# Performance work log

Measured on AMD Instinct MI355X. Metric: run time of the kernel, lower is better.

## Reference

```python
import jax, jax.numpy as jnp
import numpy as np

E, K, H, I = 16, 4, 2048, 1024
B, S = 1, 2048


def setup_inputs() -> dict:
    key = jax.random.key(0)
    ks = jax.random.split(key, 5)
    scale_in = 1.0 / np.sqrt(H)
    scale_mid = 1.0 / np.sqrt(I)
    return {
        "x": jax.random.normal(ks[0], (B, S, H), dtype=jnp.float32),
        "gate_w": jax.random.normal(ks[1], (E, H), dtype=jnp.float32) * scale_in,
        "w1_gate": jax.random.normal(ks[2], (E, I, H), dtype=jnp.float32) * scale_in,
        "w1_up": jax.random.normal(ks[3], (E, I, H), dtype=jnp.float32) * scale_in,
        "w2": jax.random.normal(ks[4], (E, H, I), dtype=jnp.float32) * scale_mid,
        "topk": K,
    }


def reference(x, gate_w, w1_gate, w1_up, w2, topk):
    orig_shape = x.shape
    xt = x.reshape(-1, x.shape[-1])            # [T, H]
    T = xt.shape[0]
    n_exp = gate_w.shape[0]

    # Router: top-k logits, softmax over the selected k (as in the torch code).
    logits = xt @ gate_w.T                      # [T, E]
    topk_vals, topk_ids = jax.lax.top_k(logits, topk)
    topk_w = jax.nn.softmax(topk_vals, axis=-1)  # [T, K]

    # Dense per-token-per-expert combine weight; 0 for unselected experts.
    # Mathematically identical to the gather/scatter-add loop: unselected
    # experts contribute expert_out * 0.
    gate_dense = jnp.zeros((T, n_exp), dtype=xt.dtype)
    gate_dense = gate_dense.at[jnp.arange(T)[:, None], topk_ids].add(topk_w)

    # SwiGLU per expert (dense over experts; weights zero-out unused ones).
    g = jnp.einsum("th,eih->tei", xt, w1_gate)   # [T, E, I]
    u = jnp.einsum("th,eih->tei", xt, w1_up)     # [T, E, I]
    h = jax.nn.silu(g) * u                        # [T, E, I]
    out = jnp.einsum("tei,te,ehi->th", h, gate_dense, w2)  # [T, H]
    return out.reshape(orig_shape)
```

## Files before the change

### kernel.cpp

```cpp
#include <hip/hip_runtime.h>
#include <hip/hip_bf16.h>
#include <stdint.h>

#define NEXP 16
#define KSEL 4
#define HDIM 2048
#define IDIM 1024
#define TTOK 2048
#define NT1 16
#define NTB 16
#define MAXT1 80
#define MAXB1 (MAXT1 * NT1)
#define MAXTB 47
#define MAXBB (MAXTB * NTB)
#define NCVT 1024
#define NCVT1 512
#define NW8 ((NEXP * IDIM * HDIM) / 8)

typedef __attribute__((ext_vector_type(8))) short bf16x8;
typedef __attribute__((ext_vector_type(4))) float f32x4;
typedef unsigned int u32;

__device__ __forceinline__ uint32_t pack2(float a, float b) {
  __hip_bfloat162 h = __float22bfloat162_rn(float2{a, b});
  uint32_t u;
  __builtin_memcpy(&u, &h, 4);
  return u;
}
__device__ __forceinline__ ushort bf1(float a) {
  __hip_bfloat16 h = __float2bfloat16(a);
  ushort u;
  __builtin_memcpy(&u, &h, 2);
  return u;
}
__device__ __forceinline__ void gload16(const void* g, void* l) {
  __builtin_amdgcn_global_load_lds(
      (const __attribute__((address_space(1))) u32*)g,
      (__attribute__((address_space(3))) u32*)l, 16, 0, 0);
}
__device__ __forceinline__ int swzread(int row, int q) {
  return row * 32 + ((q ^ ((row >> 1) & 3)) << 3);
}
__device__ __forceinline__ void cvt_bodyN(const float* __restrict__ src,
                                          ushort* __restrict__ dst,
                                          int idx0, int stride) {
  for (int i = idx0; i < NW8; i += stride) {
    f32x4 a = __builtin_nontemporal_load(((const f32x4*)src) + i * 2);
    f32x4 b = __builtin_nontemporal_load(((const f32x4*)src) + i * 2 + 1);
    uint4 t;
    t.x = pack2(a[0], a[1]); t.y = pack2(a[2], a[3]);
    t.z = pack2(b[0], b[1]); t.w = pack2(b[2], b[3]);
    ((uint4*)dst)[i] = t;
  }
}

__global__ __launch_bounds__(256) void router_kernel(
    const float* __restrict__ x, const float* __restrict__ gw,
    ushort* __restrict__ xb, int* __restrict__ topk_id,
    float* __restrict__ topk_w,
    const float* __restrict__ srcG, ushort* __restrict__ dstG,
    const float* __restrict__ srcU, ushort* __restrict__ dstU)
{
  if (blockIdx.x >= TTOK / 4 + NCVT) {
    cvt_bodyN(srcU, dstU,
              (blockIdx.x - (TTOK / 4 + NCVT)) * 256 + threadIdx.x, NCVT * 256);
    return;
  }
  if (blockIdx.x >= TTOK / 4) {
    cvt_bodyN(srcG, dstG,
              (blockIdx.x - TTOK / 4) * 256 + threadIdx.x, NCVT * 256);
    return;
  }
  const int wid = threadIdx.x >> 6;
  const int lane = threadIdx.x & 63;
  const int t = blockIdx.x * 4 + wid;
  const float4* x4 = (const float4*)(x + (size_t)t * HDIM);
  const float4* gw4 = (const float4*)gw;
  float acc[NEXP];
#pragma unroll
  for (int e = 0; e < NEXP; ++e) acc[e] = 0.f;
#pragma unroll
  for (int i = 0; i < HDIM / 256; ++i) {
    const int idx = i * 64 + lane;
    float4 xv = x4[idx];
    uint2 xp;
    xp.x = pack2(xv.x, xv.y);
    xp.y = pack2(xv.z, xv.w);
    *(uint2*)(xb + (size_t)t * HDIM + idx * 4) = xp;
#pragma unroll
    for (int e = 0; e < NEXP; ++e) {
      float4 wv = gw4[e * (HDIM / 4) + idx];
      acc[e] += xv.x * wv.x + xv.y * wv.y + xv.z * wv.z + xv.w * wv.w;
    }
  }
#pragma unroll
  for (int e = 0; e < NEXP; ++e) {
#pragma unroll
    for (int off = 32; off >= 1; off >>= 1)
      acc[e] += __shfl_xor(acc[e], off);
  }
  if (lane == 0) {
    unsigned taken = 0;
    float vals[KSEL];
    int ids[KSEL];
#pragma unroll
    for (int k = 0; k < KSEL; ++k) {
      float bv = -3.4e38f; int bi = 0;
      for (int e = 0; e < NEXP; ++e)
        if (!((taken >> e) & 1u) && acc[e] > bv) { bv = acc[e]; bi = e; }
      taken |= 1u << bi; vals[k] = bv; ids[k] = bi;
    }
    float m = vals[0], s = 0.f, w[KSEL];
#pragma unroll
    for (int k = 0; k < KSEL; ++k) { w[k] = __expf(vals[k] - m); s += w[k]; }
    float is = 1.f / s;
#pragma unroll
    for (int k = 0; k < KSEL; ++k) {
      topk_id[t * KSEL + k] = ids[k];
      topk_w[t * KSEL + k] = w[k] * is;
    }
  }
}

__global__ __launch_bounds__(1024) void plan_scatter_kernel(
    const int* __restrict__ topk_id, int* __restrict__ counts,
    int* __restrict__ offsets, int* __restrict__ nWA, int* __restrict__ nWB,
    int* __restrict__ wlA, int* __restrict__ wlB,
    int* __restrict__ rowTok, int* __restrict__ inv)
{
  __shared__ int cnt[NEXP], off[NEXP], cur[NEXP];
  __shared__ int t1[NEXP], p1[NEXP], tB[NEXP], pB[NEXP];
  const int tid = threadIdx.x;
  if (tid < NEXP) { cnt[tid] = 0; cur[tid] = 0; }
  __syncthreads();
  for (int i = tid; i < TTOK * KSEL; i += 1024)
    atomicAdd(&cnt[topk_id[i]], 1);
  __syncthreads();
  if (tid == 0) {
    int s = 0, a = 0, b = 0;
    for (int e = 0; e < NEXP; ++e) {
      off[e] = s; s += cnt[e];
      t1[e] = (cnt[e] + 127) >> 7;  p1[e] = a;  a += t1[e];
      tB[e] = (cnt[e] + 255) >> 8;  pB[e] = b;  b += tB[e];
    }
    *nWA = a * NT1;
    *nWB = b * NTB;
  }
  __syncthreads();
  if (tid < NEXP) {
    counts[tid] = cnt[tid];
    offsets[tid] = off[tid];
    const int e = tid, T = t1[e];
    int idx = p1[e] * NT1;
    for (int nt = 0; nt < NT1; ++nt)
      for (int mt = 0; mt < T; ++mt)
        wlA[idx++] = (e << 12) | (nt << 6) | mt;
  } else if (tid < 2 * NEXP) {
    const int e = tid - NEXP, T = tB[e];
    int idx = pB[e] * NTB;
    for (int nt = 0; nt < NTB; ++nt)
      for (int mt = 0; mt < T; ++mt)
        wlB[idx++] = (e << 12) | (nt << 6) | mt;
  }
  for (int i = tid; i < TTOK * KSEL; i += 1024) {
    const int e = topk_id[i];
    const int pos = atomicAdd(&cur[e], 1);
    const int row = off[e] + pos;
    rowTok[row] = i >> 2;
    inv[i] = row;
  }
}

__global__ __launch_bounds__(512) void gemm1_kernel(
    const ushort* __restrict__ xb,
    const ushort* __restrict__ wG, const ushort* __restrict__ wU,
    const int* __restrict__ rowTok, const int* __restrict__ counts,
    const int* __restrict__ offsets, const int* __restrict__ nW,
    const int* __restrict__ wl, ushort* __restrict__ hbuf,
    const float* __restrict__ cvsrc, ushort* __restrict__ cvdst)
{
  if (blockIdx.x >= MAXB1) {
    cvt_bodyN(cvsrc, cvdst,
              (blockIdx.x - MAXB1) * 512 + threadIdx.x, NCVT1 * 512);
    return;
  }
  const int nTot = *nW;
  const int L = (blockIdx.x & 7) * (MAXB1 / 8) + (blockIdx.x >> 3);
  if (L >= nTot) return;
  const int w = wl[L];
  const int e = w >> 12, nt = (w >> 6) & 63, mt = w & 63;
  const int n_e = counts[e], rowbase = offsets[e];

  __shared__ ushort lds[24576];
#define AS(b) (lds + (b) * 4096)
#define BG(b) (lds + 12288 + (b) * 2048)
#define BU(b) (lds + 18432 + (b) * 2048)

  const int tid = threadIdx.x;
  const int lane = tid & 63;
  const int wv = tid >> 6;

  const int arow = tid >> 2;
  const int ckA = tid & 3;
  const int schA = (ckA ^ ((arow >> 1) & 3)) << 3;
  const int agr = mt * 128 + arow;
  const int tokA = rowTok[rowbase + (agr < n_e ? agr : n_e - 1)];
  const ushort* pA = xb + (size_t)tokA * HDIM + schA;
  const int bloc = tid & 255;
  const int brow = bloc >> 2;
  const int ckB = bloc & 3;
  const int schB = (ckB ^ ((brow >> 1) & 3)) << 3;
  const size_t wbase = (size_t)e * IDIM * HDIM;
  const ushort* pB = ((tid < 256) ? wG : wU) + wbase +
                     (size_t)(nt * 64 + brow) * HDIM + schB;

  const int wr = (wv >> 2) << 6;
  const int ng = wv & 3;
  const bool isU = ng >= 2;
  const int wc = (ng & 1) << 5;
  const int lr = lane & 15;
  const int q = lane >> 4;

  f32x4 acc[4][2];
#pragma unroll
  for (int i = 0; i < 4; ++i)
#pragma unroll
    for (int j = 0; j < 2; ++j) acc[i][j] = (f32x4){0.f, 0.f, 0.f, 0.f};

  auto STAGE = [&](int b) {
    gload16(pA, AS(b) + tid * 8);
    if (tid < 256) gload16(pB, BG(b) + bloc * 8);
    else           gload16(pB, BU(b) + bloc * 8);
    pA += 32; pB += 32;
  };

  const int NTK = HDIM / 32;
  STAGE(0);
  STAGE(1);
  asm volatile("s_waitcnt vmcnt(2)" ::: "memory");
  __builtin_amdgcn_s_barrier();
  __builtin_amdgcn_sched_barrier(0);
  int buf = 0;
  for (int kt = 0; kt < NTK; ++kt) {
    if (kt + 2 < NTK) STAGE(buf == 0 ? 2 : buf - 1);
    const ushort* bsrc = isU ? BU(buf) : BG(buf);
    bf16x8 af[4], bf[2];
#pragma unroll
    for (int mi = 0; mi < 4; ++mi)
      af[mi] = *(const bf16x8*)&AS(buf)[swzread(wr + mi * 16 + lr, q)];
#pragma unroll
    for (int ni = 0; ni < 2; ++ni)
      bf[ni] = *(const bf16x8*)&bsrc[swzread(wc + ni * 16 + lr, q)];
#pragma unroll
    for (int mi = 0; mi < 4; ++mi)
#pragma unroll
      for (int ni = 0; ni < 2; ++ni)
        acc[mi][ni] = __builtin_amdgcn_mfma_f32_16x16x32_bf16(af[mi], bf[ni], acc[mi][ni], 0, 0, 0);
    if (kt + 1 < NTK) {
      if (kt + 2 < NTK)
        asm volatile("s_waitcnt vmcnt(2)" ::: "memory");
      else
        asm volatile("s_waitcnt vmcnt(0)" ::: "memory");
      __builtin_amdgcn_s_barrier();
      __builtin_amdgcn_sched_barrier(0);
    }
    buf = (buf == 2) ? 0 : buf + 1;
  }

  __syncthreads();
  float* uex = (float*)lds;
  if (isU) {
    const int ucol0 = ((ng - 2) << 5);
#pragma unroll
    for (int mi = 0; mi < 4; ++mi)
#pragma unroll
      for (int ni = 0; ni < 2; ++ni)
#pragma unroll
        for (int r = 0; r < 4; ++r)
          uex[(wr + mi * 16 + q * 4 + r) * 64 + ucol0 + ni * 16 + lr] = acc[mi][ni][r];
  }
  __syncthreads();
  if (!isU) {
    const int gcol0 = (ng << 5);
#pragma unroll
    for (int mi = 0; mi < 4; ++mi)
#pragma unroll
      for (int ni = 0; ni < 2; ++ni) {
        const int lcol = gcol0 + ni * 16 + lr;
        const int col = nt * 64 + lcol;
#pragma unroll
        for (int r = 0; r < 4; ++r) {
          const int lrow = wr + mi * 16 + q * 4 + r;
          const int mrow = mt * 128 + lrow;
          if (mrow < n_e) {
            const float gv = acc[mi][ni][r];
            const float uv = uex[lrow * 64 + lcol];
            const float hv = (gv / (1.f + __expf(-gv))) * uv;
            hbuf[(size_t)(rowbase + mrow) * IDIM + col] = bf1(hv);
          }
        }
      }
  }
#undef AS
#undef BG
#undef BU
}

__global__ __launch_bounds__(512) void gemmB_kernel(
    const ushort* __restrict__ hb, const ushort* __restrict__ wb,
    const int* __restrict__ counts, const int* __restrict__ offsets,
    const int* __restrict__ nW, const int* __restrict__ wl,
    ushort* __restrict__ po)
{
  const int nTot = *nW;
  const int L = (blockIdx.x & 7) * (MAXBB / 8) + (blockIdx.x >> 3);
  if (L >= nTot) return;
  const int w = wl[L];
  const int e = w >> 12, nt = (w >> 6) & 63, mt = w & 63;
  const int n_e = counts[e], rowbase = offsets[e];

  __shared__ ushort As[2][256 * 32];
  __shared__ ushort Bs[2][128 * 32];

  const int tid = threadIdx.x;
  const int lane = tid & 63;
  const int wid = tid >> 6;

  const int lr4 = lane >> 2;
  const int ckA = lane & 3;
  const int arl0 = wid * 32 + lr4;
  const int arl1 = wid * 32 + 16 + lr4;
  const int schA0 = (ckA ^ ((arl0 >> 1) & 3)) << 3;
  const int schA1 = (ckA ^ ((arl1 >> 1) & 3)) << 3;
  const int ag0 = mt * 256 + arl0, ag1 = mt * 256 + arl1;
  const int g0 = rowbase + (ag0 < n_e ? ag0 : n_e - 1);
  const int g1 = rowbase + (ag1 < n_e ? ag1 : n_e - 1);
  const ushort* pA0 = hb + (size_t)g0 * IDIM + schA0;
  const ushort* pA1 = hb + (size_t)g1 * IDIM + schA1;
  const int brl = wid * 16 + lr4;
  const int schB = (ckA ^ ((brl >> 1) & 3)) << 3;
  const size_t wbase = (size_t)e * HDIM * IDIM;
  const ushort* pB = wb + wbase + (size_t)(nt * 128 + brl) * IDIM + schB;

  const int wr = (wid >> 1) << 6;
  const int wc = (wid & 1) << 6;
  const int lr = lane & 15;
  const int q = lane >> 4;

  f32x4 acc[4][4];
#pragma unroll
  for (int i = 0; i < 4; ++i)
#pragma unroll
    for (int j = 0; j < 4; ++j) acc[i][j] = (f32x4){0.f, 0.f, 0.f, 0.f};

  auto STAGE = [&](int b) {
    gload16(pA0, &As[b][wid * 1024 + lane * 8]);
    gload16(pA1, &As[b][wid * 1024 + 512 + lane * 8]);
    gload16(pB, &Bs[b][wid * 512 + lane * 8]);
    pA0 += 32; pA1 += 32; pB += 32;
  };

  const int NTK = IDIM / 32;
  STAGE(0);
  __syncthreads();
  int buf = 0;
  for (int kt = 0; kt < NTK; ++kt) {
    if (kt + 1 < NTK) STAGE(buf ^ 1);
    bf16x8 af[4], bfr[4];
#pragma unroll
    for (int mi = 0; mi < 4; ++mi)
      af[mi] = *(const bf16x8*)&As[buf][swzread(wr + mi * 16 + lr, q)];
#pragma unroll
    for (int ni = 0; ni < 4; ++ni)
      bfr[ni] = *(const bf16x8*)&Bs[buf][swzread(wc + ni * 16 + lr, q)];
#pragma unroll
    for (int mi = 0; mi < 4; ++mi)
#pragma unroll
      for (int ni = 0; ni < 4; ++ni)
        acc[mi][ni] = __builtin_amdgcn_mfma_f32_16x16x32_bf16(af[mi], bfr[ni], acc[mi][ni], 0, 0, 0);
    __syncthreads();
    buf ^= 1;
  }

#pragma unroll
  for (int mi = 0; mi < 4; ++mi) {
#pragma unroll
    for (int ni = 0; ni < 4; ++ni) {
      const int col = nt * 128 + wc + ni * 16 + lr;
#pragma unroll
      for (int r = 0; r < 4; ++r) {
        const int mrow = mt * 256 + wr + mi * 16 + q * 4 + r;
        if (mrow < n_e)
          po[(size_t)(rowbase + mrow) * HDIM + col] = bf1(acc[mi][ni][r]);
      }
    }
  }
}

__global__ __launch_bounds__(256) void combine_kernel(
    const ushort* __restrict__ po, const int* __restrict__ inv,
    const float* __restrict__ tw, float* __restrict__ out)
{
  const int t = blockIdx.x;
  const int r0 = inv[t * 4 + 0], r1 = inv[t * 4 + 1];
  const int r2 = inv[t * 4 + 2], r3 = inv[t * 4 + 3];
  const float w0 = tw[t * 4 + 0], w1 = tw[t * 4 + 1];
  const float w2v = tw[t * 4 + 2], w3 = tw[t * 4 + 3];
  const int i = threadIdx.x;
  uint4 v0 = *(const uint4*)(po + (size_t)r0 * HDIM + i * 8);
  uint4 v1 = *(const uint4*)(po + (size_t)r1 * HDIM + i * 8);
  uint4 v2 = *(const uint4*)(po + (size_t)r2 * HDIM + i * 8);
  uint4 v3 = *(const uint4*)(po + (size_t)r3 * HDIM + i * 8);
  float o[8];
#pragma unroll
  for (int w = 0; w < 4; ++w) {
    const uint32_t a = (&v0.x)[w], b = (&v1.x)[w], c = (&v2.x)[w], d = (&v3.x)[w];
    o[w * 2 + 0] = w0 * __builtin_bit_cast(float, a << 16) +
                   w1 * __builtin_bit_cast(float, b << 16) +
                   w2v * __builtin_bit_cast(float, c << 16) +
                   w3 * __builtin_bit_cast(float, d << 16);
    o[w * 2 + 1] = w0 * __builtin_bit_cast(float, a & 0xffff0000u) +
                   w1 * __builtin_bit_cast(float, b & 0xffff0000u) +
                   w2v * __builtin_bit_cast(float, c & 0xffff0000u) +
                   w3 * __builtin_bit_cast(float, d & 0xffff0000u);
  }
  float4* o4 = (float4*)(out + (size_t)t * HDIM + i * 8);
  o4[0] = (float4){o[0], o[1], o[2], o[3]};
  o4[1] = (float4){o[4], o[5], o[6], o[7]};
}

extern "C" void kernel_launch(void* const* d_in, const int* in_sizes, int n_in,
                              void* d_out, int out_size, void* d_ws, size_t ws_size,
                              hipStream_t stream) {
  const float* x   = (const float*)d_in[0];
  const float* gw  = (const float*)d_in[1];
  const float* w1g = (const float*)d_in[2];
  const float* w1u = (const float*)d_in[3];
  const float* w2  = (const float*)d_in[4];
  float* out = (float*)d_out;

  char* ws = (char*)d_ws;
  ushort* xb    = (ushort*)(ws + 0);
  ushort* wbufG = (ushort*)(ws + 8388608);
  ushort* wbufU = (ushort*)(ws + 75497472);
  ushort* wbuf2 = (ushort*)(ws + 142606336);
  ushort* hbuf  = (ushort*)(ws + 209715200);
  ushort* po    = (ushort*)(ws + 226492416);
  int*    tkid   = (int*)(ws + 260046848);
  float*  tkw    = (float*)(ws + 260046848 + 32768);
  int*    rowTok = (int*)(ws + 260046848 + 65536);
  int*    inv    = (int*)(ws + 260046848 + 98304);
  int*    ctrl   = (int*)(ws + 260177920);
  int* counts  = ctrl;
  int* offsets = ctrl + 32;
  int* nWA     = ctrl + 50;
  int* nWB     = ctrl + 51;
  int* wlA     = ctrl + 64;
  int* wlB     = ctrl + 64 + MAXB1;

  router_kernel<<<TTOK / 4 + 2 * NCVT, 256, 0, stream>>>(
      x, gw, xb, tkid, tkw, w1g, wbufG, w1u, wbufU);
  plan_scatter_kernel<<<1, 1024, 0, stream>>>(tkid, counts, offsets, nWA, nWB,
                                              wlA, wlB, rowTok, inv);
  gemm1_kernel<<<MAXB1 + NCVT1, 512, 0, stream>>>(
      xb, wbufG, wbufU, rowTok, counts, offsets, nWA, wlA, hbuf,
      w2, wbuf2);
  gemmB_kernel<<<MAXBB, 512, 0, stream>>>(hbuf, wbuf2, counts, offsets,
                                          nWB, wlB, po);
  combine_kernel<<<TTOK, 256, 0, stream>>>(po, inv, tkw, out);
}
```

Before: 309.4 us.

## Convert fp32 gate/up weights to bf16 inside gemm1 instead of separate pass

```diff
diff --git a/kernel.cpp b/kernel.cpp
--- a/kernel.cpp
+++ b/kernel.cpp
@@ -14,7 +14,6 @@
 #define MAXTB 47
 #define MAXBB (MAXTB * NTB)
 #define NCVT 1024
-#define NCVT1 512
 #define NW8 ((NEXP * IDIM * HDIM) / 8)
 
 typedef __attribute__((ext_vector_type(8))) short bf16x8;
@@ -58,16 +57,10 @@
     const float* __restrict__ x, const float* __restrict__ gw,
     ushort* __restrict__ xb, int* __restrict__ topk_id,
     float* __restrict__ topk_w,
-    const float* __restrict__ srcG, ushort* __restrict__ dstG,
-    const float* __restrict__ srcU, ushort* __restrict__ dstU)
+    const float* __restrict__ src2, ushort* __restrict__ dst2)
 {
-  if (blockIdx.x >= TTOK / 4 + NCVT) {
-    cvt_bodyN(srcU, dstU,
-              (blockIdx.x - (TTOK / 4 + NCVT)) * 256 + threadIdx.x, NCVT * 256);
-    return;
-  }
   if (blockIdx.x >= TTOK / 4) {
-    cvt_bodyN(srcG, dstG,
+    cvt_bodyN(src2, dst2,
               (blockIdx.x - TTOK / 4) * 256 + threadIdx.x, NCVT * 256);
     return;
   }
@@ -173,17 +166,11 @@
 
 __global__ __launch_bounds__(512) void gemm1_kernel(
     const ushort* __restrict__ xb,
-    const ushort* __restrict__ wG, const ushort* __restrict__ wU,
+    const float* __restrict__ wG, const float* __restrict__ wU,
     const int* __restrict__ rowTok, const int* __restrict__ counts,
     const int* __restrict__ offsets, const int* __restrict__ nW,
-    const int* __restrict__ wl, ushort* __restrict__ hbuf,
-    const float* __restrict__ cvsrc, ushort* __restrict__ cvdst)
+    const int* __restrict__ wl, ushort* __restrict__ hbuf)
 {
-  if (blockIdx.x >= MAXB1) {
-    cvt_bodyN(cvsrc, cvdst,
-              (blockIdx.x - MAXB1) * 512 + threadIdx.x, NCVT1 * 512);
-    return;
-  }
   const int nTot = *nW;
   const int L = (blockIdx.x & 7) * (MAXB1 / 8) + (blockIdx.x >> 3);
   if (L >= nTot) return;
@@ -206,13 +193,15 @@
   const int agr = mt * 128 + arow;
   const int tokA = rowTok[rowbase + (agr < n_e ? agr : n_e - 1)];
   const ushort* pA = xb + (size_t)tokA * HDIM + schA;
+
   const int bloc = tid & 255;
-  const int brow = bloc >> 2;
+  const int browB = bloc >> 2;
   const int ckB = bloc & 3;
-  const int schB = (ckB ^ ((brow >> 1) & 3)) << 3;
-  const size_t wbase = (size_t)e * IDIM * HDIM;
-  const ushort* pB = ((tid < 256) ? wG : wU) + wbase +
-                     (size_t)(nt * 64 + brow) * HDIM + schB;
+  const int ckW = ckB ^ ((browB >> 1) & 3);
+  const size_t wbaseF = (size_t)e * IDIM * HDIM;
+  const float* pBf = ((tid < 256) ? wG : wU) + wbaseF +
+                     (size_t)(nt * 64 + browB) * HDIM + ckB * 8;
+  const int bofs = browB * 32 + ckW * 8;
 
   const int wr = (wv >> 2) << 6;
   const int ng = wv & 3;
@@ -227,44 +216,96 @@
 #pragma unroll
     for (int j = 0; j < 2; ++j) acc[i][j] = (f32x4){0.f, 0.f, 0.f, 0.f};
 
-  auto STAGE = [&](int b) {
-    gload16(pA, AS(b) + tid * 8);
-    if (tid < 256) gload16(pB, BG(b) + bloc * 8);
-    else           gload16(pB, BU(b) + bloc * 8);
-    pA += 32; pB += 32;
+  auto WRB = [&](int b, const f32x4& va, const f32x4& vb) {
+    uint4 t;
+    t.x = pack2(va[0], va[1]); t.y = pack2(va[2], va[3]);
+    t.z = pack2(vb[0], vb[1]); t.w = pack2(vb[2], vb[3]);
+    ushort* dst = (tid < 256 ? BG(b) : BU(b)) + bofs;
+    *(uint4*)dst = t;
   };
 
   const int NTK = HDIM / 32;
-  STAGE(0);
-  STAGE(1);
-  asm volatile("s_waitcnt vmcnt(2)" ::: "memory");
+  gload16(pA, AS(0) + tid * 8); pA += 32;
+  gload16(pA, AS(1) + tid * 8); pA += 32;
+  f32x4 s0a = *(const f32x4*)(pBf);
+  f32x4 s0b = *(const f32x4*)(pBf + 4);
+  WRB(0, s0a, s0b);
+  f32x4 s1a = *(const f32x4*)(pBf + 32);
+  f32x4 s1b = *(const f32x4*)(pBf + 36);
+  asm volatile("s_waitcnt lgkmcnt(0)" ::: "memory");
   __builtin_amdgcn_s_barrier();
   __builtin_amdgcn_sched_barrier(0);
-  int buf = 0;
-  for (int kt = 0; kt < NTK; ++kt) {
-    if (kt + 2 < NTK) STAGE(buf == 0 ? 2 : buf - 1);
-    const ushort* bsrc = isU ? BU(buf) : BG(buf);
-    bf16x8 af[4], bf[2];
-#pragma unroll
-    for (int mi = 0; mi < 4; ++mi)
-      af[mi] = *(const bf16x8*)&AS(buf)[swzread(wr + mi * 16 + lr, q)];
-#pragma unroll
-    for (int ni = 0; ni < 2; ++ni)
-      bf[ni] = *(const bf16x8*)&bsrc[swzread(wc + ni * 16 + lr, q)];
-#pragma unroll
-    for (int mi = 0; mi < 4; ++mi)
+
+  int cur = 0;
+  for (int t = 0; t < NTK; t += 2) {
+    {
+      const int nxt = (cur == 2) ? 0 : cur + 1;
+      const int nn = (nxt == 2) ? 0 : nxt + 1;
+      if (t + 1 < NTK) WRB(nxt, s1a, s1b);
+      if (t + 2 < NTK) {
+        s0a = *(const f32x4*)(pBf + (t + 2) * 32);
+        s0b = *(const f32x4*)(pBf + (t + 2) * 32 + 4);
+        gload16(pA, AS(nn) + tid * 8); pA += 32;
+      }
+      const ushort* bsrc = isU ? BU(cur) : BG(cur);
+      bf16x8 af[4], bf[2];
+#pragma unroll
+      for (int mi = 0; mi < 4; ++mi)
+        af[mi] = *(const bf16x8*)&AS(cur)[swzread(wr + mi * 16 + lr, q)];
 #pragma unroll
       for (int ni = 0; ni < 2; ++ni)
-        acc[mi][ni] = __builtin_amdgcn_mfma_f32_16x16x32_bf16(af[mi], bf[ni], acc[mi][ni], 0, 0, 0);
-    if (kt + 1 < NTK) {
-      if (kt + 2 < NTK)
-        asm volatile("s_waitcnt vmcnt(2)" ::: "memory");
-      else
-        asm volatile("s_waitcnt vmcnt(0)" ::: "memory");
-      __builtin_amdgcn_s_barrier();
-      __builtin_amdgcn_sched_barrier(0);
-    }
-    buf = (buf == 2) ? 0 : buf + 1;
+        bf[ni] = *(const bf16x8*)&bsrc[swzread(wc + ni * 16 + lr, q)];
+#pragma unroll
+      for (int mi = 0; mi < 4; ++mi)
+#pragma unroll
+        for (int ni = 0; ni < 2; ++ni)
+          acc[mi][ni] = __builtin_amdgcn_mfma_f32_16x16x32_bf16(af[mi], bf[ni], acc[mi][ni], 0, 0, 0);
+      if (t + 1 < NTK) {
+        if (t + 2 < NTK)
+          asm volatile("s_waitcnt vmcnt(3)" ::: "memory");
+        else
+          asm volatile("s_waitcnt vmcnt(0)" ::: "memory");
+        asm volatile("s_waitcnt lgkmcnt(0)" ::: "memory");
+        __builtin_amdgcn_s_barrier();
+        __builtin_amdgcn_sched_barrier(0);
+      }
+      cur = nxt;
+    }
+    {
+      const int u = t + 1;
+      if (u >= NTK) break;
+      const int nxt = (cur == 2) ? 0 : cur + 1;
+      const int nn = (nxt == 2) ? 0 : nxt + 1;
+      if (u + 1 < NTK) WRB(nxt, s0a, s0b);
+      if (u + 2 < NTK) {
+        s1a = *(const f32x4*)(pBf + (u + 2) * 32);
+        s1b = *(const f32x4*)(pBf + (u + 2) * 32 + 4);
+        gload16(pA, AS(nn) + tid * 8); pA += 32;
+      }
+      const ushort* bsrc = isU ? BU(cur) : BG(cur);
+      bf16x8 af[4], bf[2];
+#pragma unroll
+      for (int mi = 0; mi < 4; ++mi)
+        af[mi] = *(const bf16x8*)&AS(cur)[swzread(wr + mi * 16 + lr, q)];
+#pragma unroll
+      for (int ni = 0; ni < 2; ++ni)
+        bf[ni] = *(const bf16x8*)&bsrc[swzread(wc + ni * 16 + lr, q)];
+#pragma unroll
+      for (int mi = 0; mi < 4; ++mi)
+#pragma unroll
+        for (int ni = 0; ni < 2; ++ni)
+          acc[mi][ni] = __builtin_amdgcn_mfma_f32_16x16x32_bf16(af[mi], bf[ni], acc[mi][ni], 0, 0, 0);
+      if (u + 1 < NTK) {
+        if (u + 2 < NTK)
+          asm volatile("s_waitcnt vmcnt(3)" ::: "memory");
+        else
+          asm volatile("s_waitcnt vmcnt(0)" ::: "memory");
+        asm volatile("s_waitcnt lgkmcnt(0)" ::: "memory");
+        __builtin_amdgcn_s_barrier();
+        __builtin_amdgcn_sched_barrier(0);
+      }
+      cur = nxt;
+    }
   }
 
   __syncthreads();
@@ -441,8 +482,6 @@
 
   char* ws = (char*)d_ws;
   ushort* xb    = (ushort*)(ws + 0);
-  ushort* wbufG = (ushort*)(ws + 8388608);
-  ushort* wbufU = (ushort*)(ws + 75497472);
   ushort* wbuf2 = (ushort*)(ws + 142606336);
   ushort* hbuf  = (ushort*)(ws + 209715200);
   ushort* po    = (ushort*)(ws + 226492416);
@@ -458,13 +497,12 @@
   int* wlA     = ctrl + 64;
   int* wlB     = ctrl + 64 + MAXB1;
 
-  router_kernel<<<TTOK / 4 + 2 * NCVT, 256, 0, stream>>>(
-      x, gw, xb, tkid, tkw, w1g, wbufG, w1u, wbufU);
+  router_kernel<<<TTOK / 4 + NCVT, 256, 0, stream>>>(
+      x, gw, xb, tkid, tkw, w2, wbuf2);
   plan_scatter_kernel<<<1, 1024, 0, stream>>>(tkid, counts, offsets, nWA, nWB,
                                               wlA, wlB, rowTok, inv);
-  gemm1_kernel<<<MAXB1 + NCVT1, 512, 0, stream>>>(
-      xb, wbufG, wbufU, rowTok, counts, offsets, nWA, wlA, hbuf,
-      w2, wbuf2);
+  gemm1_kernel<<<MAXB1, 512, 0, stream>>>(
+      xb, w1g, w1u, rowTok, counts, offsets, nWA, wlA, hbuf);
   gemmB_kernel<<<MAXBB, 512, 0, stream>>>(hbuf, wbuf2, counts, offsets,
                                           nWB, wlB, po);
   combine_kernel<<<TTOK, 256, 0, stream>>>(po, inv, tkw, out);
```

New measurement: 326.9 us. 5.7% more time.
